# Kernel optimization log

Hardware: AMD Instinct MI355X
Metric: run time of the kernel (lower is better)

Reference implementation:

```python
import jax, jax.numpy as jnp
import numpy as np

DIM = 2048
H = 16           # n_heads
KV = 4           # n_kv_heads
G = H // KV      # gqa factor
CQ = 128         # q_compressed_dim
QN, QR = 96, 32  # q nope / rope head dims
CKV = 128        # kv_compressed_dim
KN, KR = 64, 64  # k nope / rope head dims
VD = 256         # v_head_dim
THETA = 10000.0


def _t5_layer_norm(x, gamma, eps=1e-5):
    mu = jnp.mean(x, axis=-1, keepdims=True)
    var = jnp.var(x, axis=-1, keepdims=True)
    return (x - mu) * jax.lax.rsqrt(var + eps) * gamma


def _rope(x):
    # x: [B, H, S, D] with interleaved even/odd rotation, positions = arange(S)
    S, D = x.shape[-2], x.shape[-1]
    inv_freq = 1.0 / THETA ** (jnp.arange(0, D, 2, dtype=jnp.float32) / D)
    ang = jnp.arange(S, dtype=jnp.float32)[:, None] * inv_freq  # [S, D/2]
    cos = jnp.cos(ang).astype(x.dtype)
    sin = jnp.sin(ang).astype(x.dtype)
    xe, xo = x[..., ::2], x[..., 1::2]
    re = xe * cos - xo * sin
    ro = xe * sin + xo * cos
    return jnp.stack((re, ro), axis=-1).reshape(x.shape)


def setup_inputs() -> dict:
    key = jax.random.key(0)
    ks = jax.random.split(key, 7)
    s = 0.02
    return {
        "x": jax.random.normal(ks[0], (2, 2048, DIM), dtype=jnp.float32),
        "w_dq": jax.random.normal(ks[1], (DIM, CQ), dtype=jnp.float32) * s,
        "gamma_q": jnp.ones((CQ,), dtype=jnp.float32),
        "w_uq": jax.random.normal(ks[2], (CQ, H * (QN + QR)), dtype=jnp.float32) * s,
        "w_dkv": jax.random.normal(ks[3], (DIM, CKV + KR), dtype=jnp.float32) * s,
        "gamma_kv": jnp.ones((CKV,), dtype=jnp.float32),
        "w_ukv": jax.random.normal(ks[4], (CKV, KV * (KN + VD)), dtype=jnp.float32) * s,
        "w_o": jax.random.normal(ks[5], (H * VD, DIM), dtype=jnp.float32) * s,
    }


def reference(x, w_dq, gamma_q, w_uq, w_dkv, gamma_kv, w_ukv, w_o):
    B, S, _ = x.shape
    # low-rank Q path
    cq = _t5_layer_norm(x @ w_dq, gamma_q)                     # [B,S,CQ]
    q = cq @ w_uq                                              # [B,S,H*(QN+QR)]
    q_nope = q[..., : H * QN].reshape(B, S, H, QN).transpose(0, 2, 1, 3)
    q_rope = q[..., H * QN :].reshape(B, S, H, QR).transpose(0, 2, 1, 3)
    q_rope = _rope(q_rope)
    q_states = jnp.concatenate((q_nope, q_rope), axis=-1)      # [B,H,S,QN+QR]

    # low-rank KV path + decoupled shared rope key
    ckv_kr = x @ w_dkv                                         # [B,S,CKV+KR]
    ckv = _t5_layer_norm(ckv_kr[..., :CKV], gamma_kv)
    k_rope = _rope(ckv_kr[..., CKV:][:, None, :, :])           # [B,1,S,KR]
    kv = ckv @ w_ukv                                           # [B,S,KV*(KN+VD)]
    k_nope = kv[..., : KV * KN].reshape(B, S, KV, KN).transpose(0, 2, 1, 3)
    v_states = kv[..., KV * KN :].reshape(B, S, KV, VD).transpose(0, 2, 1, 3)
    k_states = jnp.concatenate(
        (k_nope, jnp.broadcast_to(k_rope, (B, KV, S, KR))), axis=-1
    )                                                          # [B,KV,S,KN+KR]

    # grouped-query attention: broadcast kv heads instead of materializing repeats
    dqk = QN + QR  # == KN + KR == 128
    qg = q_states.reshape(B, KV, G, S, dqk)
    scores = jnp.einsum("bgrqd,bgkd->bgrqk", qg, k_states) / jnp.sqrt(
        jnp.asarray(dqk, dtype=x.dtype)
    )
    causal = jnp.triu(jnp.ones((S, S), dtype=bool), k=1)
    scores = jnp.where(causal, -jnp.inf, scores)
    attn = jax.nn.softmax(scores, axis=-1)
    out = jnp.einsum("bgrqk,bgkv->bgrqv", attn, v_states)      # [B,KV,G,S,VD]
    out = out.reshape(B, H, S, VD).transpose(0, 2, 1, 3).reshape(B, S, H * VD)
    return out @ w_o
```

## Files before the change

kernel.cpp:

```cpp
#include <hip/hip_runtime.h>
#include <hip/hip_bf16.h>
#include <math.h>

#define DIM   2048
#define S_LEN 2048
#define BATCH 2
#define NH    16
#define NKV   4
#define CQ_   128
#define QN_   96
#define QR_   32
#define CKV_  128
#define KN_   64
#define KR_   64
#define VD_   256
#define DQK   192
#define DV    128
#define ROWS_TOT (BATCH*S_LEN)
#define QK_SCALE 0.08838834764831845f
#define LOG2E    1.4426950408889634f

typedef __attribute__((ext_vector_type(8)))  short short8;
typedef __attribute__((ext_vector_type(4)))  short short4v;
typedef __attribute__((ext_vector_type(4)))  float float4v;
typedef __attribute__((ext_vector_type(16))) float float16v;
typedef __attribute__((ext_vector_type(4)))  int   int4v;

__device__ inline short f2bf(float x) {
    union { __hip_bfloat16 h; short s; } u;
    u.h = __float2bfloat16(x);
    return u.s;
}

__device__ __forceinline__ void gl_lds16(const short* g, short* lds) {
    __builtin_amdgcn_global_load_lds(
        (const __attribute__((address_space(1))) unsigned int*)(g),
        (__attribute__((address_space(3))) unsigned int*)(lds),
        16, 0, 0);
}

__device__ __forceinline__ short8 cast8(const float* p) {
    float4 a = *reinterpret_cast<const float4*>(p);
    float4 b = *reinterpret_cast<const float4*>(p + 4);
    short8 o;
    o[0] = f2bf(a.x); o[1] = f2bf(a.y); o[2] = f2bf(a.z); o[3] = f2bf(a.w);
    o[4] = f2bf(b.x); o[5] = f2bf(b.y); o[6] = f2bf(b.z); o[7] = f2bf(b.w);
    return o;
}


__global__ __launch_bounds__(256)
void kprep_all(const float* __restrict__ w_o, const float* __restrict__ w_uq,
               const float* __restrict__ w_dq, const float* __restrict__ w_dkv,
               short* __restrict__ w_oT, short* __restrict__ w_uqT,
               short* __restrict__ wdT, float* __restrict__ tq,
               float* __restrict__ tk)
{
    const int bid = blockIdx.x, tid = threadIdx.x;
    if (bid >= 2272) {
        int gid = (bid - 2272) * 256 + tid;
        int spos = gid / 48, e = gid - spos * 48;
        if (e < 16) {
            float inv = powf(10000.f, -(float)(2 * e) / 32.f);
            float sn, c; sincosf((float)spos * inv, &sn, &c);
            tq[(spos * 16 + e) * 2 + 0] = c;
            tq[(spos * 16 + e) * 2 + 1] = sn;
        } else {
            int i2 = e - 16;
            float inv = powf(10000.f, -(float)(2 * i2) / 64.f);
            float sn, c; sincosf((float)spos * inv, &sn, &c);
            tk[(spos * 32 + i2) * 2 + 0] = c;
            tk[(spos * 32 + i2) * 2 + 1] = sn;
        }
        return;
    }

    __shared__ float tf[64][65];
    int lb, nct, R; short* dst;
    if (bid < 160)      { lb = bid;       nct = 5;  R = 2048; dst = wdT;   }
    else if (bid < 224) { lb = bid - 160; nct = 32; R = 128;  dst = w_uqT; }
    else                { lb = bid - 224; nct = 32; R = 4096; dst = w_oT;  }
    const int ct = lb % nct, rt = lb / nct;
    const int r0 = rt * 64, c0 = ct * 64;
    const float* src; int stride, nbase;
    if (bid < 160) {
        if (ct < 2) { src = w_dq;  stride = 128; nbase = c0; }
        else        { src = w_dkv; stride = 192; nbase = c0 - 128; }
    } else if (bid < 224) { src = w_uq; stride = 2048; nbase = c0; }
    else                  { src = w_o;  stride = 2048; nbase = c0; }

    #pragma unroll
    for (int u4 = 0; u4 < 4; ++u4) {
        int u = u4 * 256 + tid;
        int kr = u >> 4, nc = (u & 15) * 4;
        float4 v = *reinterpret_cast<const float4*>(&src[(size_t)(r0 + kr) * stride + nbase + nc]);
        tf[kr][nc + 0] = v.x; tf[kr][nc + 1] = v.y;
        tf[kr][nc + 2] = v.z; tf[kr][nc + 3] = v.w;
    }
    __syncthreads();
    #pragma unroll
    for (int u2 = 0; u2 < 2; ++u2) {
        int u = u2 * 256 + tid;
        int nr = u >> 3, kc8 = (u & 7) * 8;
        short8 o;
        #pragma unroll
        for (int j = 0; j < 8; ++j) o[j] = f2bf(tf[kc8 + j][nr]);
        *reinterpret_cast<short8*>(&dst[(size_t)(c0 + nr) * R + r0 + kc8]) = o;
    }
}

__global__ __launch_bounds__(256)
void kcomb(const float* __restrict__ w_uq, const float* __restrict__ w_ukv,
           const short* __restrict__ w_oT,
           short* __restrict__ WqcombT, short* __restrict__ WcombT)
{
    const int tid = threadIdx.x, lane = tid & 63, wid = tid >> 6;
    const int g = lane >> 4, l15 = lane & 15;

    if (blockIdx.x < 16) {
        const int h = blockIdx.x, kvh = h >> 2;
        float4v acc[2][8];
        #pragma unroll
        for (int mi = 0; mi < 2; ++mi)
            #pragma unroll
            for (int nj = 0; nj < 8; ++nj) acc[mi][nj] = (float4v){0.f, 0.f, 0.f, 0.f};
        #pragma unroll
        for (int kb = 0; kb < 2; ++kb) {
            short8 af[2], bf[8];
            #pragma unroll
            for (int mi = 0; mi < 2; ++mi) {
                int j = wid * 32 + mi * 16 + l15;
                af[mi] = cast8(&w_ukv[(size_t)j * 1280 + kvh * 64 + kb * 32 + g * 8]);
            }
            #pragma unroll
            for (int nj = 0; nj < 8; ++nj) {
                int e = nj * 16 + l15;
                bf[nj] = cast8(&w_uq[(size_t)e * 2048 + h * 96 + kb * 32 + g * 8]);
            }
            #pragma unroll
            for (int mi = 0; mi < 2; ++mi)
                #pragma unroll
                for (int nj = 0; nj < 8; ++nj)
                    acc[mi][nj] = __builtin_amdgcn_mfma_f32_16x16x32_bf16(
                        af[mi], bf[nj], acc[mi][nj], 0, 0, 0);
        }
        #pragma unroll
        for (int mi = 0; mi < 2; ++mi)
            #pragma unroll
            for (int nj = 0; nj < 8; ++nj)
                #pragma unroll
                for (int r = 0; r < 4; ++r)
                    WqcombT[(size_t)h * 16384 + (wid * 32 + mi * 16 + g * 4 + r) * 128
                            + nj * 16 + l15] = f2bf(acc[mi][nj][r]);
    } else {
        const int bb = blockIdx.x - 16;
        const int h = bb >> 4, nt = bb & 15, kvh = h >> 2;
        const int wm = wid >> 1, wn = wid & 1;
        float4v acc[4][4];
        #pragma unroll
        for (int mi = 0; mi < 4; ++mi)
            #pragma unroll
            for (int nj = 0; nj < 4; ++nj) acc[mi][nj] = (float4v){0.f, 0.f, 0.f, 0.f};
        for (int kb = 0; kb < 8; ++kb) {
            short8 af[4], bf[4];
            #pragma unroll
            for (int mi = 0; mi < 4; ++mi) {
                int n = nt * 128 + wm * 64 + mi * 16 + l15;
                af[mi] = *reinterpret_cast<const short8*>(
                    &w_oT[(size_t)n * 4096 + h * 256 + kb * 32 + g * 8]);
            }
            #pragma unroll
            for (int nj = 0; nj < 4; ++nj) {
                int c = wn * 64 + nj * 16 + l15;
                bf[nj] = cast8(&w_ukv[(size_t)c * 1280 + 256 + kvh * 256 + kb * 32 + g * 8]);
            }
            #pragma unroll
            for (int mi = 0; mi < 4; ++mi)
                #pragma unroll
                for (int nj = 0; nj < 4; ++nj)
                    acc[mi][nj] = __builtin_amdgcn_mfma_f32_16x16x32_bf16(
                        af[mi], bf[nj], acc[mi][nj], 0, 0, 0);
        }
        #pragma unroll
        for (int mi = 0; mi < 4; ++mi)
            #pragma unroll
            for (int nj = 0; nj < 4; ++nj)
                #pragma unroll
                for (int r = 0; r < 4; ++r)
                    WcombT[(size_t)(nt * 128 + wm * 64 + mi * 16 + g * 4 + r) * 2048
                           + h * 128 + wn * 64 + nj * 16 + l15] = f2bf(acc[mi][nj][r]);
    }
}

__global__ __launch_bounds__(256)
void k1_mfma(const float* __restrict__ x, const short* __restrict__ wdT,
             const float* __restrict__ gamma_q, const float* __restrict__ gamma_kv,
             const float* __restrict__ tk,
             short* __restrict__ cq_bf, short* __restrict__ kimg,
             short* __restrict__ vimg)
{
    __shared__ float ys[16][321];
    __shared__ float st[16][4];
    const int tid = threadIdx.x, lane = tid & 63, w = tid >> 6;
    const int g = lane >> 4, l15 = lane & 15;
    const int m0 = blockIdx.x * 16;
    const int wn0 = w * 80;

    float4v acc[5];
    #pragma unroll
    for (int nj = 0; nj < 5; ++nj) acc[nj] = (float4v){0.f, 0.f, 0.f, 0.f};

    const float* arow = x + (size_t)(m0 + l15) * 2048 + g * 8;
    for (int ks = 0; ks < 64; ++ks) {
        short8 a = cast8(arow + ks * 32);
        #pragma unroll
        for (int nj = 0; nj < 5; ++nj) {
            short8 bf = *reinterpret_cast<const short8*>(
                wdT + (size_t)(wn0 + nj * 16 + l15) * 2048 + ks * 32 + g * 8);
            acc[nj] = __builtin_amdgcn_mfma_f32_16x16x32_bf16(a, bf, acc[nj], 0, 0, 0);
        }
    }

    #pragma unroll
    for (int nj = 0; nj < 5; ++nj)
        #pragma unroll
        for (int r = 0; r < 4; ++r)
            ys[g * 4 + r][wn0 + nj * 16 + l15] = acc[nj][r];
    __syncthreads();

    if (tid < 32) {
        int row = tid >> 1, seg = tid & 1, base = seg * 128;
        float s1 = 0.f, s2 = 0.f;
        for (int j = 0; j < 128; ++j) { float v = ys[row][base + j]; s1 += v; s2 += v * v; }
        float mu  = s1 * (1.f / 128.f);
        float var = s2 * (1.f / 128.f) - mu * mu;
        st[row][seg * 2 + 0] = mu;
        st[row][seg * 2 + 1] = rsqrtf(var + 1e-5f);
    }
    __syncthreads();

    for (int i = tid; i < 16 * 128; i += 256) {
        int row = i >> 7, col = i & 127;
        int r = m0 + row;
        cq_bf[(size_t)r * CQ_ + col] =
            f2bf((ys[row][col] - st[row][0]) * st[row][1] * gamma_q[col] * (QK_SCALE * LOG2E));
    }
    for (int i = tid; i < 16 * 192; i += 256) {
        int row = i / 192, d = i - row * 192;
        int r = m0 + row, b = r >> 11, spos = r & (S_LEN - 1);
        int tile = b * 32 + (spos >> 6);
        float val;
        if (d < 128) {
            val = (ys[row][128 + d] - st[row][2]) * st[row][3] * gamma_kv[d];
            short v_ = f2bf(val);
            size_t vslot = (d >> 5) * 256 + ((spos >> 5) & 1) * 128
                           + ((spos >> 4) & 1) * 64 + ((spos >> 3) & 1) * 32 + (d & 31);
            vimg[((size_t)tile * 1024 + vslot) * 8 + (spos & 7)] = v_;
            size_t kslot = ((spos >> 5) & 1) * 768 + (d >> 4) * 64
                           + ((d >> 3) & 1) * 32 + (spos & 31);
            kimg[((size_t)tile * 1536 + kslot) * 8 + (d & 7)] = v_;
        } else {
            int dd = d - 128, i2 = dd >> 1;
            float xe = ys[row][256 + (dd & ~1)];
            float xo = ys[row][256 + (dd | 1)];
            float c  = tk[(spos * 32 + i2) * 2 + 0];
            float sn = tk[(spos * 32 + i2) * 2 + 1];
            val = (dd & 1) ? (xe * sn + xo * c) : (xe * c - xo * sn);
            size_t kslot = ((spos >> 5) & 1) * 768 + (d >> 4) * 64
                           + ((d >> 3) & 1) * 32 + (spos & 31);
            kimg[((size_t)tile * 1536 + kslot) * 8 + (d & 7)] = f2bf(val);
        }
    }
}

__global__ __launch_bounds__(256)
void k2_mfma(const short* __restrict__ cq_bf, const short* __restrict__ WqcombT,
             const short* __restrict__ w_uqT, const float* __restrict__ tq,
             short* __restrict__ q_states)
{
    const int tid = threadIdx.x, lane = tid & 63, w = tid >> 6;
    const int g = lane >> 4, l15 = lane & 15;
    const int bm = blockIdx.x / 3, ns = blockIdx.x % 3;
    const int m0 = bm * 16;
    const int nb = ns * 1024 + w * 256;

    short8 af[4];
    #pragma unroll
    for (int ks = 0; ks < 4; ++ks)
        af[ks] = *reinterpret_cast<const short8*>(
            cq_bf + (size_t)(m0 + l15) * 128 + ks * 32 + g * 8);

    float4v acc[16];
    #pragma unroll
    for (int nj = 0; nj < 16; ++nj) acc[nj] = (float4v){0.f, 0.f, 0.f, 0.f};

    #pragma unroll
    for (int ks = 0; ks < 4; ++ks)
        #pragma unroll
        for (int nj = 0; nj < 16; ++nj) {
            int j = nb + nj * 16 + l15;
            int h = j / 192, t = j - h * 192;
            const short* brow;
            if (t < 128)       brow = WqcombT + (size_t)h * 16384 + (size_t)t * 128;
            else if (t < 160)  brow = w_uqT + (size_t)(h * 96 + 64 + (t - 128)) * 128;
            else               brow = w_uqT + (size_t)(1536 + h * 32 + (t - 160)) * 128;
            short8 bf = *reinterpret_cast<const short8*>(brow + ks * 32 + g * 8);
            acc[nj] = __builtin_amdgcn_mfma_f32_16x16x32_bf16(af[ks], bf, acc[nj], 0, 0, 0);
        }

    #pragma unroll
    for (int nj = 0; nj < 16; ++nj) {
        int j = nb + nj * 16 + l15;
        int h = j / 192, t = j - h * 192;
        if (t < 160) {
            #pragma unroll
            for (int r = 0; r < 4; ++r) {
                int rg = m0 + g * 4 + r, bb = rg >> 11, spos = rg & (S_LEN - 1);
                q_states[((size_t)(bb * NH + h) * S_LEN + spos) * DQK + t] =
                    f2bf(acc[nj][r]);
            }
        } else {
            int dd = t - 160, i2 = dd >> 1;
            #pragma unroll
            for (int r = 0; r < 4; ++r) {
                int rg = m0 + g * 4 + r, bb = rg >> 11, spos = rg & (S_LEN - 1);
                float v = acc[nj][r];
                float p = __shfl_xor(v, 1, 64);
                float c  = tq[(spos * 16 + i2) * 2 + 0];
                float sn = tq[(spos * 16 + i2) * 2 + 1];
                float out = (dd & 1) ? (p * sn + v * c) : (v * c - p * sn);
                q_states[((size_t)(bb * NH + h) * S_LEN + spos) * DQK + t] = f2bf(out);
            }
        }
    }
}

__global__ __launch_bounds__(512, 1)
void k4_attn_mfma(const short* __restrict__ q_states,
                  const short* __restrict__ kimg,
                  const short* __restrict__ vimg,
                  short* __restrict__ attn_out)
{
    __shared__ __align__(16) short ks_lds[3][12288];
    __shared__ __align__(16) short vt_lds[2][8192];

    const int tid = threadIdx.x, lane = tid & 63, w = tid >> 6;
    const int bid = blockIdx.x;
    const int l31 = lane & 31, hi = lane >> 5;
    const int g = w & 3, h = w >> 2;
    const int qt = (bid < 256) ? (15 - (bid >> 5)) : (7 - ((bid - 256) >> 5));
    const int bh = bid & 31;
    const int h_head = bh & 15, b = bh >> 4;

    const short* kfbase = kimg + (size_t)b * 32 * 12288;
    const short* vfbase = vimg + (size_t)b * 32 * 8192;

    const int qrow0 = qt * 128 + g * 32;
    const int qglob = qrow0 + l31;

    short8 qcur[12];
    {
        const short* qr = q_states +
            ((size_t)(b * NH + h_head) * S_LEN + qglob) * DQK + hi * 8;
        #pragma unroll
        for (int st = 0; st < 12; ++st)
            qcur[st] = *reinterpret_cast<const short8*>(qr + st * 16);
    }

    float16v o[4];
    #pragma unroll
    for (int dt = 0; dt < 4; ++dt)
        #pragma unroll
        for (int r = 0; r < 16; ++r) o[dt][r] = 0.f;
    float mreg = -1e30f, lreg = 0.f;

    const int nkt = 2 * (qt + 1);

    auto issueK = [&](int kt, int bufi) {
        const short* src = kfbase + (size_t)kt * 12288;
        #pragma unroll
        for (int i = 0; i < 3; ++i) {
            int c = w * 3 + i;
            gl_lds16(src + c * 512 + lane * 8, &ks_lds[bufi][c * 512]);
        }
    };
    auto issueV = [&](int kt, int bufi) {
        const short* src = vfbase + (size_t)kt * 8192;
        #pragma unroll
        for (int i = 0; i < 2; ++i) {
            int c = w * 2 + i;
            gl_lds16(src + c * 512 + lane * 8, &vt_lds[bufi][c * 512]);
        }
    };

    issueK(0, 0);
    issueV(0, 0);
    issueK(1, 1);

    for (int seq = 0; seq < nkt; ++seq) {
        if (seq < nkt - 1) { asm volatile("s_waitcnt vmcnt(3)" ::: "memory"); }
        else               { asm volatile("s_waitcnt vmcnt(0)" ::: "memory"); }
        __builtin_amdgcn_s_barrier();
        __builtin_amdgcn_sched_barrier(0);

        if (seq + 1 < nkt) issueV(seq + 1, (seq + 1) & 1);
        if (seq + 2 < nkt) issueK(seq + 2, (seq + 2) % 3);

        const int kvb = seq * 64 + h * 32;
        if (kvb <= qrow0 + 31) {
            const short* kbuf = &ks_lds[seq % 3][h * 6144];
            float16v sa, sb;
            #pragma unroll
            for (int r = 0; r < 16; ++r) { sa[r] = 0.f; sb[r] = 0.f; }
            __builtin_amdgcn_s_setprio(1);
            #pragma unroll
            for (int st = 0; st < 12; st += 2) {
                short8 kf0 = *reinterpret_cast<const short8*>(kbuf + st * 512 + lane * 8);
                sa = __builtin_amdgcn_mfma_f32_32x32x16_bf16(kf0, qcur[st], sa, 0, 0, 0);
                short8 kf1 = *reinterpret_cast<const short8*>(kbuf + (st + 1) * 512 + lane * 8);
                sb = __builtin_amdgcn_mfma_f32_32x32x16_bf16(kf1, qcur[st + 1], sb, 0, 0, 0);
            }
            __builtin_amdgcn_s_setprio(0);
            float16v s;
            #pragma unroll
            for (int r = 0; r < 16; ++r) s[r] = sa[r] + sb[r];

            if (kvb + 31 > qrow0) {
                #pragma unroll
                for (int r = 0; r < 16; ++r) {
                    int kc = kvb + ((r & 3) + 8 * (r >> 2) + 4 * hi);
                    if (kc > qglob) s[r] = -1e30f;
                }
            }

            float mx = s[0];
            #pragma unroll
            for (int r = 1; r < 16; ++r) mx = fmaxf(mx, s[r]);
            mx = fmaxf(mx, __shfl_xor(mx, 32, 64));
            bool need = mx > mreg + 8.f;
            if (__ballot(need)) {
                float mnew = fmaxf(mreg, mx);
                float corr = exp2f(mreg - mnew);
                mreg = mnew;
                lreg *= corr;
                #pragma unroll
                for (int dt = 0; dt < 4; ++dt)
                    #pragma unroll
                    for (int r = 0; r < 16; ++r) o[dt][r] *= corr;
            }
            #pragma unroll
            for (int r = 0; r < 16; ++r) s[r] = exp2f(s[r] - mreg);
            float ps = 0.f;
            #pragma unroll
            for (int r = 0; r < 16; ++r) ps += s[r];
            ps += __shfl_xor(ps, 32, 64);
            lreg += ps;

            const short* vbuf = &vt_lds[seq & 1][h * 1024];
            __builtin_amdgcn_s_setprio(1);
            #pragma unroll
            for (int ks = 0; ks < 2; ++ks) {
                const int rb = ks * 8;
                int c01, c23, c45, c67;
                asm("v_cvt_pk_bf16_f32 %0, %1, %2" : "=v"(c01) : "v"(s[rb+0]), "v"(s[rb+1]));
                asm("v_cvt_pk_bf16_f32 %0, %1, %2" : "=v"(c23) : "v"(s[rb+2]), "v"(s[rb+3]));
                asm("v_cvt_pk_bf16_f32 %0, %1, %2" : "=v"(c45) : "v"(s[rb+4]), "v"(s[rb+5]));
                asm("v_cvt_pk_bf16_f32 %0, %1, %2" : "=v"(c67) : "v"(s[rb+6]), "v"(s[rb+7]));
                asm("v_permlane32_swap_b32 %0, %1" : "+v"(c01), "+v"(c45));
                asm("v_permlane32_swap_b32 %0, %1" : "+v"(c23), "+v"(c67));
                union { int4v i4; short8 s8; } u_;
                u_.i4.x = c01; u_.i4.y = c23; u_.i4.z = c45; u_.i4.w = c67;
                short8 pa = u_.s8;
                #pragma unroll
                for (int dt = 0; dt < 4; ++dt) {
                    short8 vf = *reinterpret_cast<const short8*>(
                        vbuf + dt * 2048 + ks * 512 + lane * 8);
                    o[dt] = __builtin_amdgcn_mfma_f32_32x32x16_bf16(vf, pa, o[dt], 0, 0, 0);
                }
            }
            __builtin_amdgcn_s_setprio(0);
        }
    }

    __syncthreads();
    {
        float* mlb = (float*)(&ks_lds[0][0]);
        mlb[w * 64 + lane] = mreg;
        mlb[512 + w * 64 + lane] = lreg;
    }
    __syncthreads();
    float s0f = 0.f, s1f = 0.f;
    if (h == 0) {
        float* mlb = (float*)(&ks_lds[0][0]);
        float m1 = mlb[(w + 4) * 64 + lane];
        float l1 = mlb[512 + (w + 4) * 64 + lane];
        float ms = fmaxf(mreg, m1);
        float c0 = exp2f(mreg - ms), c1 = exp2f(m1 - ms);
        float ls = lreg * c0 + l1 * c1;
        s0f = c0 / ls; s1f = c1 / ls;
    }
    float* cb = (float*)(&ks_lds[0][0]) + 1024;
    short* obase = attn_out + ((size_t)(b * S_LEN + qglob)) * 2048 + h_head * 128;
    for (int dt = 0; dt < 4; ++dt) {
        __syncthreads();
        if (h == 1) {
            #pragma unroll
            for (int r = 0; r < 16; ++r)
                cb[r * 256 + g * 64 + lane] = o[dt][r];
        }
        __syncthreads();
        if (h == 0) {
            #pragma unroll
            for (int r = 0; r < 16; ++r)
                o[dt][r] = o[dt][r] * s0f + cb[r * 256 + g * 64 + lane] * s1f;
            #pragma unroll
            for (int k4i = 0; k4i < 4; ++k4i) {
                int d0 = dt * 32 + k4i * 8 + hi * 4;
                short4v pk;
                #pragma unroll
                for (int j = 0; j < 4; ++j) pk[j] = f2bf(o[dt][k4i * 4 + j]);
                *reinterpret_cast<short4v*>(obase + d0) = pk;
            }
        }
    }
}

__global__ __launch_bounds__(256)
void k5_gemm_mfma(const short* __restrict__ A,
                  const short* __restrict__ Bt,
                  float* __restrict__ C)
{
    __shared__ __align__(16) short at[128 * 64];
    __shared__ __align__(16) short bt[128 * 64];
    const int tid  = threadIdx.x;
    const int lane = tid & 63;
    const int wid  = tid >> 6;
    const int wm = wid >> 1, wn = wid & 1;
    const int g = lane >> 4, l15 = lane & 15;
    const int wg = (blockIdx.x & 7) * 64 + (blockIdx.x >> 3);
    const int bn = wg & 15, bm = wg >> 4;
    const int m0 = bm * 128, n0 = bn * 128;

    float4v acc[4][4];
    #pragma unroll
    for (int mi = 0; mi < 4; ++mi)
        #pragma unroll
        for (int nj = 0; nj < 4; ++nj) acc[mi][nj] = (float4v){0.f, 0.f, 0.f, 0.f};

    for (int k0 = 0; k0 < 2048; k0 += 64) {
        __syncthreads();
        #pragma unroll
        for (int i = 0; i < 4; ++i) {
            int row = wid * 32 + i * 8 + (lane >> 3);
            int ch  = lane & 7;
            gl_lds16(A + (size_t)(m0 + row) * 2048 + k0 + ((ch ^ (row & 7)) * 8),
                     at + wid * 2048 + i * 512);
            gl_lds16(Bt + (size_t)(n0 + row) * 2048 + k0 + ((ch ^ (row & 7)) * 8),
                     bt + wid * 2048 + i * 512);
        }
        __syncthreads();

        #pragma unroll
        for (int kb = 0; kb < 2; ++kb) {
            short8 af[4], bfr[4];
            #pragma unroll
            for (int mi = 0; mi < 4; ++mi) {
                int row = wm * 64 + mi * 16 + l15;
                af[mi] = *reinterpret_cast<const short8*>(
                    at + row * 64 + (((g + 4 * kb) ^ (row & 7)) * 8));
            }
            #pragma unroll
            for (int nj = 0; nj < 4; ++nj) {
                int row = wn * 64 + nj * 16 + l15;
                bfr[nj] = *reinterpret_cast<const short8*>(
                    bt + row * 64 + (((g + 4 * kb) ^ (row & 7)) * 8));
            }
            #pragma unroll
            for (int mi = 0; mi < 4; ++mi)
                #pragma unroll
                for (int nj = 0; nj < 4; ++nj)
                    acc[mi][nj] = __builtin_amdgcn_mfma_f32_16x16x32_bf16(
                        af[mi], bfr[nj], acc[mi][nj], 0, 0, 0);
        }
    }

    #pragma unroll
    for (int mi = 0; mi < 4; ++mi)
        #pragma unroll
        for (int nj = 0; nj < 4; ++nj)
            #pragma unroll
            for (int r = 0; r < 4; ++r)
                C[(size_t)(m0 + wm * 64 + mi * 16 + g * 4 + r) * DIM + n0 + wn * 64 + nj * 16 + l15] =
                    acc[mi][nj][r];
}

extern "C" void kernel_launch(void* const* d_in, const int* in_sizes, int n_in,
                              void* d_out, int out_size, void* d_ws, size_t ws_size,
                              hipStream_t stream)
{
    const float* x        = (const float*)d_in[0];
    const float* w_dq     = (const float*)d_in[1];
    const float* gamma_q  = (const float*)d_in[2];
    const float* w_uq     = (const float*)d_in[3];
    const float* w_dkv    = (const float*)d_in[4];
    const float* gamma_kv = (const float*)d_in[5];
    const float* w_ukv    = (const float*)d_in[6];
    const float* w_o      = (const float*)d_in[7];
    float* out = (float*)d_out;

    char* ws = (char*)d_ws;
    short* cq_bf    = (short*)(ws);
    float* tq       = (float*)(ws + (1ull  << 20));
    float* tk       = (float*)(ws + (2ull  << 20));
    short* w_uqT    = (short*)(ws + (3ull  << 20));
    short* wdT      = (short*)(ws + (4ull  << 20));
    short* WqcombT  = (short*)(ws + (6ull  << 20));
    short* kimg     = (short*)(ws + (7ull  << 20));
    short* vimg     = (short*)(ws + (9ull  << 20));
    short* q_states = (short*)(ws + (11ull << 20));
    short* attn_out = (short*)(ws + (38ull << 20));
    short* w_oT     = (short*)(ws + (54ull << 20));
    short* WcombT   = (short*)(ws + (70ull << 20));

    kprep_all<<<dim3(2656), dim3(256), 0, stream>>>(
        w_o, w_uq, w_dq, w_dkv, w_oT, w_uqT, wdT, tq, tk);

    kcomb<<<dim3(272), dim3(256), 0, stream>>>(
        w_uq, w_ukv, w_oT, WqcombT, WcombT);

    k1_mfma<<<dim3(ROWS_TOT / 16), dim3(256), 0, stream>>>(
        x, wdT, gamma_q, gamma_kv, tk, cq_bf, kimg, vimg);

    k2_mfma<<<dim3((ROWS_TOT / 16) * 3), dim3(256), 0, stream>>>(
        cq_bf, WqcombT, w_uqT, tq, q_states);

    k4_attn_mfma<<<dim3(512), dim3(512), 0, stream>>>(
        q_states, kimg, vimg, attn_out);

    k5_gemm_mfma<<<dim3(512), dim3(256), 0, stream>>>(
        attn_out, WcombT, out);
}
```

Baseline: 236.1 us.

## Fuse weight prep kernels and merge Q down/up projection kernels

Merges the weight-transpose and weight-combine kernels into a single launch. The w_o transpose is no longer written to global memory; instead each combine block loads and transposes its own w_o tile into LDS. Also fuses the down-projection/layernorm kernel with the Q up-projection kernel, so cq stays in LDS rather than making a global round trip. This removes two launches and some global traffic, but the fused k12 block now does three times the up-projection work with a larger shared footprint, and the prep kernel reserves 66KB of LDS in every block, including the small-table blocks, which may limit occupancy.

Result: slower. 252.4 us (+6.9%).

```diff
diff --git a/kernel.cpp b/kernel.cpp
--- a/kernel.cpp
+++ b/kernel.cpp
@@ -48,17 +48,54 @@
     return o;
 }
 
-
 __global__ __launch_bounds__(256)
-void kprep_all(const float* __restrict__ w_o, const float* __restrict__ w_uq,
-               const float* __restrict__ w_dq, const float* __restrict__ w_dkv,
-               short* __restrict__ w_oT, short* __restrict__ w_uqT,
-               short* __restrict__ wdT, float* __restrict__ tq,
-               float* __restrict__ tk)
+void kw_prep(const float* __restrict__ w_o, const float* __restrict__ w_uq,
+             const float* __restrict__ w_ukv, const float* __restrict__ w_dq,
+             const float* __restrict__ w_dkv,
+             short* __restrict__ wdT, short* __restrict__ w_uqT,
+             short* __restrict__ WqcombT, short* __restrict__ WcombT,
+             float* __restrict__ tq, float* __restrict__ tk)
 {
+    __shared__ char smem[67584];
     const int bid = blockIdx.x, tid = threadIdx.x;
-    if (bid >= 2272) {
-        int gid = (bid - 2272) * 256 + tid;
+    const int lane = tid & 63, wid = tid >> 6;
+    const int g = lane >> 4, l15 = lane & 15;
+
+    if (bid < 224) {
+        float* tf = (float*)smem;
+        int lb, nct, R; short* dst;
+        if (bid < 160) { lb = bid;       nct = 5;  R = 2048; dst = wdT;   }
+        else           { lb = bid - 160; nct = 32; R = 128;  dst = w_uqT; }
+        const int ct = lb % nct, rt = lb / nct;
+        const int r0 = rt * 64, c0 = ct * 64;
+        const float* src; int stride, nbase;
+        if (bid < 160) {
+            if (ct < 2) { src = w_dq;  stride = 128; nbase = c0; }
+            else        { src = w_dkv; stride = 192; nbase = c0 - 128; }
+        } else { src = w_uq; stride = 2048; nbase = c0; }
+
+        #pragma unroll
+        for (int u4 = 0; u4 < 4; ++u4) {
+            int u = u4 * 256 + tid;
+            int kr = u >> 4, nc = (u & 15) * 4;
+            float4 v = *reinterpret_cast<const float4*>(&src[(size_t)(r0 + kr) * stride + nbase + nc]);
+            tf[kr * 65 + nc + 0] = v.x; tf[kr * 65 + nc + 1] = v.y;
+            tf[kr * 65 + nc + 2] = v.z; tf[kr * 65 + nc + 3] = v.w;
+        }
+        __syncthreads();
+        #pragma unroll
+        for (int u2 = 0; u2 < 2; ++u2) {
+            int u = u2 * 256 + tid;
+            int nr = u >> 3, kc8 = (u & 7) * 8;
+            short8 o;
+            #pragma unroll
+            for (int j = 0; j < 8; ++j) o[j] = f2bf(tf[(kc8 + j) * 65 + nr]);
+            *reinterpret_cast<short8*>(&dst[(size_t)(c0 + nr) * R + r0 + kc8]) = o;
+        }
+        return;
+    }
+    if (bid < 608) {
+        int gid = (bid - 224) * 256 + tid;
         int spos = gid / 48, e = gid - spos * 48;
         if (e < 16) {
             float inv = powf(10000.f, -(float)(2 * e) / 32.f);
@@ -74,51 +111,8 @@
         }
         return;
     }
-
-    __shared__ float tf[64][65];
-    int lb, nct, R; short* dst;
-    if (bid < 160)      { lb = bid;       nct = 5;  R = 2048; dst = wdT;   }
-    else if (bid < 224) { lb = bid - 160; nct = 32; R = 128;  dst = w_uqT; }
-    else                { lb = bid - 224; nct = 32; R = 4096; dst = w_oT;  }
-    const int ct = lb % nct, rt = lb / nct;
-    const int r0 = rt * 64, c0 = ct * 64;
-    const float* src; int stride, nbase;
-    if (bid < 160) {
-        if (ct < 2) { src = w_dq;  stride = 128; nbase = c0; }
-        else        { src = w_dkv; stride = 192; nbase = c0 - 128; }
-    } else if (bid < 224) { src = w_uq; stride = 2048; nbase = c0; }
-    else                  { src = w_o;  stride = 2048; nbase = c0; }
-
-    #pragma unroll
-    for (int u4 = 0; u4 < 4; ++u4) {
-        int u = u4 * 256 + tid;
-        int kr = u >> 4, nc = (u & 15) * 4;
-        float4 v = *reinterpret_cast<const float4*>(&src[(size_t)(r0 + kr) * stride + nbase + nc]);
-        tf[kr][nc + 0] = v.x; tf[kr][nc + 1] = v.y;
-        tf[kr][nc + 2] = v.z; tf[kr][nc + 3] = v.w;
-    }
-    __syncthreads();
-    #pragma unroll
-    for (int u2 = 0; u2 < 2; ++u2) {
-        int u = u2 * 256 + tid;
-        int nr = u >> 3, kc8 = (u & 7) * 8;
-        short8 o;
-        #pragma unroll
-        for (int j = 0; j < 8; ++j) o[j] = f2bf(tf[kc8 + j][nr]);
-        *reinterpret_cast<short8*>(&dst[(size_t)(c0 + nr) * R + r0 + kc8]) = o;
-    }
-}
-
-__global__ __launch_bounds__(256)
-void kcomb(const float* __restrict__ w_uq, const float* __restrict__ w_ukv,
-           const short* __restrict__ w_oT,
-           short* __restrict__ WqcombT, short* __restrict__ WcombT)
-{
-    const int tid = threadIdx.x, lane = tid & 63, wid = tid >> 6;
-    const int g = lane >> 4, l15 = lane & 15;
-
-    if (blockIdx.x < 16) {
-        const int h = blockIdx.x, kvh = h >> 2;
+    if (bid < 624) {
+        const int h = bid - 608, kvh = h >> 2;
         float4v acc[2][8];
         #pragma unroll
         for (int mi = 0; mi < 2; ++mi)
@@ -152,10 +146,26 @@
                 for (int r = 0; r < 4; ++r)
                     WqcombT[(size_t)h * 16384 + (wid * 32 + mi * 16 + g * 4 + r) * 128
                             + nj * 16 + l15] = f2bf(acc[mi][nj][r]);
-    } else {
-        const int bb = blockIdx.x - 16;
+        return;
+    }
+
+    {
+        const int bb = bid - 624;
         const int h = bb >> 4, nt = bb & 15, kvh = h >> 2;
         const int wm = wid >> 1, wn = wid & 1;
+        short* wot = (short*)smem;
+
+        for (int u = tid; u < 8192; u += 256) {
+            int r = u >> 5, c4 = (u & 31) * 4;
+            float4 v = *reinterpret_cast<const float4*>(
+                &w_o[(size_t)(h * 256 + r) * DIM + nt * 128 + c4]);
+            wot[(c4 + 0) * 264 + r] = f2bf(v.x);
+            wot[(c4 + 1) * 264 + r] = f2bf(v.y);
+            wot[(c4 + 2) * 264 + r] = f2bf(v.z);
+            wot[(c4 + 3) * 264 + r] = f2bf(v.w);
+        }
+        __syncthreads();
+
         float4v acc[4][4];
         #pragma unroll
         for (int mi = 0; mi < 4; ++mi)
@@ -165,9 +175,9 @@
             short8 af[4], bf[4];
             #pragma unroll
             for (int mi = 0; mi < 4; ++mi) {
-                int n = nt * 128 + wm * 64 + mi * 16 + l15;
+                int nl = wm * 64 + mi * 16 + l15;
                 af[mi] = *reinterpret_cast<const short8*>(
-                    &w_oT[(size_t)n * 4096 + h * 256 + kb * 32 + g * 8]);
+                    &wot[nl * 264 + kb * 32 + g * 8]);
             }
             #pragma unroll
             for (int nj = 0; nj < 4; ++nj) {
@@ -193,22 +203,24 @@
 }
 
 __global__ __launch_bounds__(256)
-void k1_mfma(const float* __restrict__ x, const short* __restrict__ wdT,
-             const float* __restrict__ gamma_q, const float* __restrict__ gamma_kv,
-             const float* __restrict__ tk,
-             short* __restrict__ cq_bf, short* __restrict__ kimg,
-             short* __restrict__ vimg)
+void k12_mfma(const float* __restrict__ x, const short* __restrict__ wdT,
+              const float* __restrict__ gamma_q, const float* __restrict__ gamma_kv,
+              const float* __restrict__ tk, const float* __restrict__ tq,
+              const short* __restrict__ WqcombT, const short* __restrict__ w_uqT,
+              short* __restrict__ kimg, short* __restrict__ vimg,
+              short* __restrict__ q_states)
 {
     __shared__ float ys[16][321];
     __shared__ float st[16][4];
+    __shared__ short cqs[16][136];
     const int tid = threadIdx.x, lane = tid & 63, w = tid >> 6;
     const int g = lane >> 4, l15 = lane & 15;
     const int m0 = blockIdx.x * 16;
     const int wn0 = w * 80;
 
-    float4v acc[5];
+    float4v acc5[5];
     #pragma unroll
-    for (int nj = 0; nj < 5; ++nj) acc[nj] = (float4v){0.f, 0.f, 0.f, 0.f};
+    for (int nj = 0; nj < 5; ++nj) acc5[nj] = (float4v){0.f, 0.f, 0.f, 0.f};
 
     const float* arow = x + (size_t)(m0 + l15) * 2048 + g * 8;
     for (int ks = 0; ks < 64; ++ks) {
@@ -217,7 +229,7 @@
         for (int nj = 0; nj < 5; ++nj) {
             short8 bf = *reinterpret_cast<const short8*>(
                 wdT + (size_t)(wn0 + nj * 16 + l15) * 2048 + ks * 32 + g * 8);
-            acc[nj] = __builtin_amdgcn_mfma_f32_16x16x32_bf16(a, bf, acc[nj], 0, 0, 0);
+            acc5[nj] = __builtin_amdgcn_mfma_f32_16x16x32_bf16(a, bf, acc5[nj], 0, 0, 0);
         }
     }
 
@@ -225,7 +237,7 @@
     for (int nj = 0; nj < 5; ++nj)
         #pragma unroll
         for (int r = 0; r < 4; ++r)
-            ys[g * 4 + r][wn0 + nj * 16 + l15] = acc[nj][r];
+            ys[g * 4 + r][wn0 + nj * 16 + l15] = acc5[nj][r];
     __syncthreads();
 
     if (tid < 32) {
@@ -241,17 +253,15 @@
 
     for (int i = tid; i < 16 * 128; i += 256) {
         int row = i >> 7, col = i & 127;
-        int r = m0 + row;
-        cq_bf[(size_t)r * CQ_ + col] =
+        cqs[row][col] =
             f2bf((ys[row][col] - st[row][0]) * st[row][1] * gamma_q[col] * (QK_SCALE * LOG2E));
     }
     for (int i = tid; i < 16 * 192; i += 256) {
         int row = i / 192, d = i - row * 192;
         int r = m0 + row, b = r >> 11, spos = r & (S_LEN - 1);
         int tile = b * 32 + (spos >> 6);
-        float val;
         if (d < 128) {
-            val = (ys[row][128 + d] - st[row][2]) * st[row][3] * gamma_kv[d];
+            float val = (ys[row][128 + d] - st[row][2]) * st[row][3] * gamma_kv[d];
             short v_ = f2bf(val);
             size_t vslot = (d >> 5) * 256 + ((spos >> 5) & 1) * 128
                            + ((spos >> 4) & 1) * 64 + ((spos >> 3) & 1) * 32 + (d & 31);
@@ -265,71 +275,62 @@
             float xo = ys[row][256 + (dd | 1)];
             float c  = tk[(spos * 32 + i2) * 2 + 0];
             float sn = tk[(spos * 32 + i2) * 2 + 1];
-            val = (dd & 1) ? (xe * sn + xo * c) : (xe * c - xo * sn);
+            float val = (dd & 1) ? (xe * sn + xo * c) : (xe * c - xo * sn);
             size_t kslot = ((spos >> 5) & 1) * 768 + (d >> 4) * 64
                            + ((d >> 3) & 1) * 32 + (spos & 31);
             kimg[((size_t)tile * 1536 + kslot) * 8 + (d & 7)] = f2bf(val);
         }
     }
-}
-
-__global__ __launch_bounds__(256)
-void k2_mfma(const short* __restrict__ cq_bf, const short* __restrict__ WqcombT,
-             const short* __restrict__ w_uqT, const float* __restrict__ tq,
-             short* __restrict__ q_states)
-{
-    const int tid = threadIdx.x, lane = tid & 63, w = tid >> 6;
-    const int g = lane >> 4, l15 = lane & 15;
-    const int bm = blockIdx.x / 3, ns = blockIdx.x % 3;
-    const int m0 = bm * 16;
-    const int nb = ns * 1024 + w * 256;
+    __syncthreads();
 
     short8 af[4];
     #pragma unroll
     for (int ks = 0; ks < 4; ++ks)
-        af[ks] = *reinterpret_cast<const short8*>(
-            cq_bf + (size_t)(m0 + l15) * 128 + ks * 32 + g * 8);
-
-    float4v acc[16];
-    #pragma unroll
-    for (int nj = 0; nj < 16; ++nj) acc[nj] = (float4v){0.f, 0.f, 0.f, 0.f};
-
-    #pragma unroll
-    for (int ks = 0; ks < 4; ++ks)
+        af[ks] = *reinterpret_cast<const short8*>(&cqs[l15][ks * 32 + g * 8]);
+
+    for (int ns = 0; ns < 3; ++ns) {
+        const int nb = ns * 1024 + w * 256;
+        float4v acc[16];
+        #pragma unroll
+        for (int nj = 0; nj < 16; ++nj) acc[nj] = (float4v){0.f, 0.f, 0.f, 0.f};
+
+        #pragma unroll
+        for (int ks = 0; ks < 4; ++ks)
+            #pragma unroll
+            for (int nj = 0; nj < 16; ++nj) {
+                int j = nb + nj * 16 + l15;
+                int h = j / 192, t = j - h * 192;
+                const short* brow;
+                if (t < 128)       brow = WqcombT + (size_t)h * 16384 + (size_t)t * 128;
+                else if (t < 160)  brow = w_uqT + (size_t)(h * 96 + 64 + (t - 128)) * 128;
+                else               brow = w_uqT + (size_t)(1536 + h * 32 + (t - 160)) * 128;
+                short8 bf = *reinterpret_cast<const short8*>(brow + ks * 32 + g * 8);
+                acc[nj] = __builtin_amdgcn_mfma_f32_16x16x32_bf16(af[ks], bf, acc[nj], 0, 0, 0);
+            }
+
         #pragma unroll
         for (int nj = 0; nj < 16; ++nj) {
             int j = nb + nj * 16 + l15;
             int h = j / 192, t = j - h * 192;
-            const short* brow;
-            if (t < 128)       brow = WqcombT + (size_t)h * 16384 + (size_t)t * 128;
-            else if (t < 160)  brow = w_uqT + (size_t)(h * 96 + 64 + (t - 128)) * 128;
-            else               brow = w_uqT + (size_t)(1536 + h * 32 + (t - 160)) * 128;
-            short8 bf = *reinterpret_cast<const short8*>(brow + ks * 32 + g * 8);
-            acc[nj] = __builtin_amdgcn_mfma_f32_16x16x32_bf16(af[ks], bf, acc[nj], 0, 0, 0);
-        }
-
-    #pragma unroll
-    for (int nj = 0; nj < 16; ++nj) {
-        int j = nb + nj * 16 + l15;
-        int h = j / 192, t = j - h * 192;
-        if (t < 160) {
-            #pragma unroll
-            for (int r = 0; r < 4; ++r) {
-                int rg = m0 + g * 4 + r, bb = rg >> 11, spos = rg & (S_LEN - 1);
-                q_states[((size_t)(bb * NH + h) * S_LEN + spos) * DQK + t] =
-                    f2bf(acc[nj][r]);
-            }
-        } else {
-            int dd = t - 160, i2 = dd >> 1;
-            #pragma unroll
-            for (int r = 0; r < 4; ++r) {
-                int rg = m0 + g * 4 + r, bb = rg >> 11, spos = rg & (S_LEN - 1);
-                float v = acc[nj][r];
-                float p = __shfl_xor(v, 1, 64);
-                float c  = tq[(spos * 16 + i2) * 2 + 0];
-                float sn = tq[(spos * 16 + i2) * 2 + 1];
-                float out = (dd & 1) ? (p * sn + v * c) : (v * c - p * sn);
-                q_states[((size_t)(bb * NH + h) * S_LEN + spos) * DQK + t] = f2bf(out);
+            if (t < 160) {
+                #pragma unroll
+                for (int r = 0; r < 4; ++r) {
+                    int rg = m0 + g * 4 + r, bb = rg >> 11, spos = rg & (S_LEN - 1);
+                    q_states[((size_t)(bb * NH + h) * S_LEN + spos) * DQK + t] =
+                        f2bf(acc[nj][r]);
+                }
+            } else {
+                int dd = t - 160, i2 = dd >> 1;
+                #pragma unroll
+                for (int r = 0; r < 4; ++r) {
+                    int rg = m0 + g * 4 + r, bb = rg >> 11, spos = rg & (S_LEN - 1);
+                    float v = acc[nj][r];
+                    float p = __shfl_xor(v, 1, 64);
+                    float c  = tq[(spos * 16 + i2) * 2 + 0];
+                    float sn = tq[(spos * 16 + i2) * 2 + 1];
+                    float out = (dd & 1) ? (p * sn + v * c) : (v * c - p * sn);
+                    q_states[((size_t)(bb * NH + h) * S_LEN + spos) * DQK + t] = f2bf(out);
+                }
             }
         }
     }
@@ -609,30 +610,22 @@
     float* out = (float*)d_out;
 
     char* ws = (char*)d_ws;
-    short* cq_bf    = (short*)(ws);
-    float* tq       = (float*)(ws + (1ull  << 20));
-    float* tk       = (float*)(ws + (2ull  << 20));
-    short* w_uqT    = (short*)(ws + (3ull  << 20));
-    short* wdT      = (short*)(ws + (4ull  << 20));
-    short* WqcombT  = (short*)(ws + (6ull  << 20));
-    short* kimg     = (short*)(ws + (7ull  << 20));
-    short* vimg     = (short*)(ws + (9ull  << 20));
-    short* q_states = (short*)(ws + (11ull << 20));
-    short* attn_out = (short*)(ws + (38ull << 20));
-    short* w_oT     = (short*)(ws + (54ull << 20));
-    short* WcombT   = (short*)(ws + (70ull << 20));
-
-    kprep_all<<<dim3(2656), dim3(256), 0, stream>>>(
-        w_o, w_uq, w_dq, w_dkv, w_oT, w_uqT, wdT, tq, tk);
-
-    kcomb<<<dim3(272), dim3(256), 0, stream>>>(
-        w_uq, w_ukv, w_oT, WqcombT, WcombT);
-
-    k1_mfma<<<dim3(ROWS_TOT / 16), dim3(256), 0, stream>>>(
-        x, wdT, gamma_q, gamma_kv, tk, cq_bf, kimg, vimg);
-
-    k2_mfma<<<dim3((ROWS_TOT / 16) * 3), dim3(256), 0, stream>>>(
-        cq_bf, WqcombT, w_uqT, tq, q_states);
+    float* tq       = (float*)(ws);
+    float* tk       = (float*)(ws + (1ull  << 20));
+    short* w_uqT    = (short*)(ws + (2ull  << 20));
+    short* wdT      = (short*)(ws + (3ull  << 20));
+    short* WqcombT  = (short*)(ws + (5ull  << 20));
+    short* kimg     = (short*)(ws + (6ull  << 20));
+    short* vimg     = (short*)(ws + (8ull  << 20));
+    short* q_states = (short*)(ws + (10ull << 20));
+    short* attn_out = (short*)(ws + (36ull << 20));
+    short* WcombT   = (short*)(ws + (52ull << 20));
+
+    kw_prep<<<dim3(880), dim3(256), 0, stream>>>(
+        w_o, w_uq, w_ukv, w_dq, w_dkv, wdT, w_uqT, WqcombT, WcombT, tq, tk);
+
+    k12_mfma<<<dim3(ROWS_TOT / 16), dim3(256), 0, stream>>>(
+        x, wdT, gamma_q, gamma_kv, tk, tq, WqcombT, w_uqT, kimg, vimg, q_states);
 
     k4_attn_mfma<<<dim3(512), dim3(512), 0, stream>>>(
         q_states, kimg, vimg, attn_out);
```
